# Kernel tuning notes

Hardware: AMD Instinct MI355X
Metric: run time of the kernel (lower is better)

## Reference

```python
import jax, jax.numpy as jnp
import numpy as np

B, C, H, W = 16, 256, 32, 32
N_HEAD, DIM_HEAD = 8, 32  # dim_hidden = 256 == C


def setup_inputs() -> dict:
    key = jax.random.key(0)
    ks = jax.random.split(key, 9)
    s = 1.0 / np.sqrt(C)
    return {
        "x": jax.random.normal(ks[0], (B, C, H, W), dtype=jnp.float32),
        "w_q": jax.random.normal(ks[1], (C, C), dtype=jnp.float32) * s,
        "b_q": jnp.zeros((C,), dtype=jnp.float32),
        "w_k": jax.random.normal(ks[2], (C, C), dtype=jnp.float32) * s,
        "b_k": jnp.zeros((C,), dtype=jnp.float32),
        "w_v": jax.random.normal(ks[3], (C, C), dtype=jnp.float32) * s,
        "b_v": jnp.zeros((C,), dtype=jnp.float32),
        "w_o": jax.random.normal(ks[4], (C, C), dtype=jnp.float32) * s,
        "b_o": jnp.zeros((C,), dtype=jnp.float32),
    }


def reference(x, w_q, b_q, w_k, b_k, w_v, b_v, w_o, b_o):
    b, c, h, w = x.shape
    L = h * w
    scale = DIM_HEAD ** (-0.5)
    xf = x.reshape(b, c, L)  # [b, c, L]

    def proj(wm, bm):
        # 1x1 conv == per-position linear over channels
        y = jnp.einsum('oc,bcl->bol', wm, xf) + bm[None, :, None]
        return y.reshape(b, N_HEAD, DIM_HEAD, L)

    q = proj(w_q, b_q) * scale
    k = proj(w_k, b_k)
    v = proj(w_v, b_v)

    sim = jnp.einsum('bndl,bndm->bnlm', q, k)           # [b, n, L, L]
    att = jax.nn.softmax(sim, axis=-1)
    out = jnp.einsum('bnlm,bndm->bndl', att, v)         # [b, n, d, L]
    out = out.reshape(b, c, L)
    out = jnp.einsum('oc,bcl->bol', w_o, out) + b_o[None, :, None]
    return out.reshape(b, c, h, w)
```

## Files before the change

### kernel.cpp

```cpp
#include <hip/hip_runtime.h>
#include <hip/hip_bf16.h>
#include <math.h>

namespace {
constexpr int B_ = 16, C_ = 256, L_ = 1024, NH_ = 8, DH_ = 32;

typedef __attribute__((ext_vector_type(8))) short short8v;
typedef __attribute__((ext_vector_type(4))) float float4v;

__device__ __forceinline__ short f2bf(float f) {
    unsigned u = __builtin_bit_cast(unsigned, f);
    u += 0x7fffu + ((u >> 16) & 1u);
    return (short)(u >> 16);
}
__device__ __forceinline__ unsigned pkrn(float a, float b) {
    float2 f; f.x = a; f.y = b;
    __hip_bfloat162 h = __float22bfloat162_rn(f);
    unsigned u;
    __builtin_memcpy(&u, &h, sizeof(u));
    return u;
}
__device__ __forceinline__ void gld16(const short* g, short* l) {
    __builtin_amdgcn_global_load_lds(
        (const __attribute__((address_space(1))) unsigned*)g,
        (__attribute__((address_space(3))) unsigned*)l, 16, 0, 0);
}

__global__ __launch_bounds__(256) void prepw_kernel(
    const float* __restrict__ wq, const float* __restrict__ wk,
    const float* __restrict__ wv, const float* __restrict__ wo,
    short* __restrict__ WA, short* __restrict__ WoA)
{
    const int g4 = blockIdx.x * 256 + threadIdx.x;
    const int o = g4 >> 6, cc = (g4 & 63) * 4;
    const float* src = (o < 256) ? wq : (o < 512) ? wk : (o < 768) ? wv : wo;
    const float4 v = *(const float4*)&src[(size_t)(o & 255) * 256 + cc];
    short4 s;
    s.x = f2bf(v.x); s.y = f2bf(v.y); s.z = f2bf(v.z); s.w = f2bf(v.w);
    short* dst = (o < 768) ? &WA[(size_t)o * 256 + cc]
                           : &WoA[(size_t)(o - 768) * 256 + cc];
    *(short4*)dst = s;
}

__global__ __launch_bounds__(256, 3) void qkv_kernel(
    const float* __restrict__ X, const short* __restrict__ WA,
    const float* __restrict__ bias0, const float* __restrict__ bias1, const float* __restrict__ bias2,
    float qscale, short* __restrict__ out0, short* __restrict__ out1, short* __restrict__ out2)
{
    const int lt = blockIdx.x, typ = blockIdx.y, b = blockIdx.z;
    const int t = threadIdx.x, wv = t >> 6, lane = t & 63;
    const int quad = lane >> 4, c = lane & 15;
    const int wo = (wv & 1) * 128;
    const int wl = (wv >> 1) * 32;

    __shared__ short sA[256 * 64];
    __shared__ short sB[64 * 64];

    float4v acc[8][2];
#pragma unroll
    for (int i = 0; i < 8; ++i)
#pragma unroll
        for (int j = 0; j < 2; ++j) acc[i][j] = (float4v)0.f;

    const short* Arow = WA + (size_t)(typ * 256) * 256;
    const int srow = t >> 3, sseg = t & 7;
    const int seg = sseg ^ (srow & 7);

    for (int kk = 0; kk < 4; ++kk) {
        __syncthreads();
#pragma unroll
        for (int e = 0; e < 8; ++e)
            gld16(Arow + (size_t)(e * 32 + srow) * 256 + kk * 64 + seg * 8,
                  &sA[(e * 256 + t) * 8]);
        {
            const int lrow = t & 63, w8 = t >> 6;
            const float* xcol = X + ((size_t)b * C_ + kk * 64 + w8 * 16) * L_ + lt * 64 + lrow;
            float vvv[16];
#pragma unroll
            for (int j = 0; j < 16; ++j) vvv[j] = xcol[(size_t)j * L_];
            unsigned pk[8];
#pragma unroll
            for (int j = 0; j < 8; ++j) pk[j] = pkrn(vvv[2 * j], vvv[2 * j + 1]);
            *(uint4*)&sB[(lrow * 8 + ((2 * w8)     ^ (lrow & 7))) * 8] = *(uint4*)&pk[0];
            *(uint4*)&sB[(lrow * 8 + ((2 * w8 + 1) ^ (lrow & 7))) * 8] = *(uint4*)&pk[4];
        }
        __syncthreads();

#pragma unroll
        for (int kc2 = 0; kc2 < 2; ++kc2) {
            short8v bf[2];
#pragma unroll
            for (int j = 0; j < 2; ++j) {
                const int row = wl + 16 * j + c;
                bf[j] = *(const short8v*)&sB[row * 64 + (((kc2 * 4 + quad) ^ (c & 7)) * 8)];
            }
#pragma unroll
            for (int half = 0; half < 2; ++half) {
                short8v af[4];
#pragma unroll
                for (int i2 = 0; i2 < 4; ++i2) {
                    const int row = wo + (half * 4 + i2) * 16 + c;
                    af[i2] = *(const short8v*)&sA[row * 64 + (((kc2 * 4 + quad) ^ (c & 7)) * 8)];
                }
#pragma unroll
                for (int i2 = 0; i2 < 4; ++i2)
#pragma unroll
                    for (int j = 0; j < 2; ++j)
                        acc[half * 4 + i2][j] = __builtin_amdgcn_mfma_f32_16x16x32_bf16(
                            af[i2], bf[j], acc[half * 4 + i2][j], 0, 0, 0);
            }
        }
    }

    const float* bp = (typ == 0) ? bias0 : (typ == 1) ? bias1 : bias2;
    const float sc = (typ == 0) ? qscale : 1.f;
    short* outp = (typ == 0) ? out0 : (typ == 1) ? out1 : out2;
    if (typ < 2) {
#pragma unroll
        for (int i = 0; i < 8; ++i) {
            const int ch0 = wo + 16 * i + quad * 4;
            const int head = ch0 >> 5, d0 = ch0 & 31;
            float bias[4];
#pragma unroll
            for (int r = 0; r < 4; ++r) bias[r] = bp[ch0 + r];
#pragma unroll
            for (int j = 0; j < 2; ++j) {
                const int l = lt * 64 + wl + 16 * j + c;
                short4 sv;
                sv.x = f2bf((acc[i][j][0] + bias[0]) * sc);
                sv.y = f2bf((acc[i][j][1] + bias[1]) * sc);
                sv.z = f2bf((acc[i][j][2] + bias[2]) * sc);
                sv.w = f2bf((acc[i][j][3] + bias[3]) * sc);
                *(short4*)&outp[(((size_t)b * NH_ + head) * L_ + l) * 32 + d0] = sv;
            }
        }
    } else {
#pragma unroll
        for (int i = 0; i < 8; ++i)
#pragma unroll
            for (int r = 0; r < 4; ++r) {
                const int ch = wo + 16 * i + quad * 4 + r;
                const float bias = bp[ch];
#pragma unroll
                for (int j = 0; j < 2; ++j)
                    outp[((size_t)b * C_ + ch) * L_ + lt * 64 + wl + 16 * j + c] =
                        f2bf(acc[i][j][r] + bias);
            }
    }
}

__global__ __launch_bounds__(256, 4) void ogemm_kernel(
    const short* __restrict__ WoA,
    const short* __restrict__ Bsrc,
    const float* __restrict__ bias,
    float* __restrict__ out)
{
    const int lt = blockIdx.x, ot = blockIdx.y, b = blockIdx.z;
    const int t = threadIdx.x, wv = t >> 6, lane = t & 63;
    const int quad = lane >> 4, c = lane & 15;
    const int wo = (wv & 1) * 64;
    const int wl = (wv >> 1) * 32;

    __shared__ short sA[128 * 64];
    __shared__ short sB[64 * 64];

    float4v acc[4][2];
#pragma unroll
    for (int i = 0; i < 4; ++i)
#pragma unroll
        for (int j = 0; j < 2; ++j) acc[i][j] = (float4v)0.f;

    const short* Arow = WoA + (size_t)(ot * 128) * 256;
    const int srow = t >> 3, sseg = t & 7;
    const int seg = sseg ^ (srow & 7);

    for (int kk = 0; kk < 4; ++kk) {
        __syncthreads();
#pragma unroll
        for (int e = 0; e < 4; ++e)
            gld16(Arow + (size_t)(e * 32 + srow) * 256 + kk * 64 + seg * 8,
                  &sA[(e * 256 + t) * 8]);
#pragma unroll
        for (int e = 0; e < 2; ++e)
            gld16(Bsrc + ((size_t)b * L_ + lt * 64 + e * 32 + srow) * 256 + kk * 64 + seg * 8,
                  &sB[(e * 256 + t) * 8]);
        __syncthreads();

#pragma unroll
        for (int kc2 = 0; kc2 < 2; ++kc2) {
            short8v af[4], bf[2];
#pragma unroll
            for (int i = 0; i < 4; ++i) {
                const int row = wo + 16 * i + c;
                af[i] = *(const short8v*)&sA[row * 64 + (((kc2 * 4 + quad) ^ (c & 7)) * 8)];
            }
#pragma unroll
            for (int j = 0; j < 2; ++j) {
                const int row = wl + 16 * j + c;
                bf[j] = *(const short8v*)&sB[row * 64 + (((kc2 * 4 + quad) ^ (c & 7)) * 8)];
            }
#pragma unroll
            for (int i = 0; i < 4; ++i)
#pragma unroll
                for (int j = 0; j < 2; ++j)
                    acc[i][j] = __builtin_amdgcn_mfma_f32_16x16x32_bf16(af[i], bf[j], acc[i][j], 0, 0, 0);
        }
    }

#pragma unroll
    for (int i = 0; i < 4; ++i)
#pragma unroll
        for (int r = 0; r < 4; ++r) {
            const int ch = ot * 128 + wo + 16 * i + quad * 4 + r;
            const float bs = bias[ch];
#pragma unroll
            for (int j = 0; j < 2; ++j)
                out[((size_t)b * C_ + ch) * L_ + lt * 64 + wl + 16 * j + c] =
                    acc[i][j][r] + bs;
        }
}

__global__ __launch_bounds__(256, 4) void attn_kernel(
    const short* __restrict__ qt,
    const short* __restrict__ kt,
    const short* __restrict__ vb,
    short* __restrict__ athi)
{
    const int flat = blockIdx.x;
    const int g = ((flat >> 6) << 3) | (flat & 7);
    const int chunk = (flat >> 3) & 7;
    const int b = g >> 3, h = g & 7;
    const int t = threadIdx.x;
    const int wv = t >> 6, lane = t & 63;
    const int quad = lane >> 4, c = lane & 15;
    const int lq0 = chunk * 128 + wv * 32;

    __shared__ __align__(16) short sK[2][64 * 32];
    __shared__ __align__(16) short sV[2][2][32 * 32];
    __shared__ __align__(16) short sPT[4][2][16][64];

    const size_t bh = (size_t)b * NH_ + h;
    const short* qbase = qt + (bh * L_) * 32;
    const short* kbase = kt + (bh * L_) * 32;
    const size_t vrow = (size_t)b * C_ + h * DH_;

    short8v qfrag[2];
#pragma unroll
    for (int qf = 0; qf < 2; ++qf)
        qfrag[qf] = *(const short8v*)(qbase + (size_t)(lq0 + qf * 16 + c) * 32 + quad * 8);

    float lp4[2][4];
#pragma unroll
    for (int qf = 0; qf < 2; ++qf)
#pragma unroll
        for (int r = 0; r < 4; ++r) lp4[qf][r] = 0.f;
    float4v o_acc[2][2];
#pragma unroll
    for (int qf = 0; qf < 2; ++qf) { o_acc[qf][0] = (float4v)0.f; o_acc[qf][1] = (float4v)0.f; }

    const int sseg = (t & 3) ^ ((t >> 3) & 3);
    const int rsw = (c >> 1) & 3;

    auto stage = [&](int m0, int buf) {
        gld16(kbase + (size_t)(m0 + (t >> 2)) * 32 + sseg * 8, &sK[buf][t * 8]);
        gld16(vb + (vrow + ((t >> 2) & 31)) * L_ + m0 + (t >> 7) * 32 + sseg * 8,
              (short*)sV[buf] + t * 8);
    };

    stage(0, 0);

    short8v vfp[2][2];

    for (int i = 0; i <= 16; ++i) {
        short8v kf[4], vf[2][2];
        if (i < 16) {
            __syncthreads();
            if (i < 15) stage((i + 1) * 64, (i + 1) & 1);
            const short* Kb = sK[i & 1];
            const short* Vb = (const short*)sV[i & 1];
#pragma unroll
            for (int kb = 0; kb < 4; ++kb)
                kf[kb] = *(const short8v*)&Kb[(kb * 16 + c) * 32 + ((quad ^ rsw) * 8)];
#pragma unroll
            for (int kc = 0; kc < 2; ++kc)
#pragma unroll
                for (int nb2 = 0; nb2 < 2; ++nb2)
                    vf[kc][nb2] = *(const short8v*)&Vb[kc * 1024 + (nb2 * 16 + c) * 32 + ((quad ^ rsw) * 8)];
        }

        if (i > 0) {
#pragma unroll
            for (int qf = 0; qf < 2; ++qf)
#pragma unroll
                for (int kc = 0; kc < 2; ++kc) {
                    const int G = (kc * 4 + quad) ^ (c & 7);
                    const short8v pf = *(const short8v*)&sPT[wv][qf][c][G * 8];
#pragma unroll
                    for (int nb2 = 0; nb2 < 2; ++nb2)
                        o_acc[qf][nb2] = __builtin_amdgcn_mfma_f32_16x16x32_bf16(vfp[kc][nb2], pf, o_acc[qf][nb2], 0, 0, 0);
                }
        }

        if (i < 16) {
            float4v st[2][4];
#pragma unroll
            for (int qf = 0; qf < 2; ++qf)
#pragma unroll
                for (int kb = 0; kb < 4; ++kb)
                    st[qf][kb] = __builtin_amdgcn_mfma_f32_16x16x32_bf16(kf[kb], qfrag[qf], (float4v)0.f, 0, 0, 0);
#pragma unroll
            for (int qf = 0; qf < 2; ++qf)
#pragma unroll
                for (int kb = 0; kb < 4; ++kb) {
                    float p[4];
#pragma unroll
                    for (int r = 0; r < 4; ++r) {
                        p[r] = __builtin_amdgcn_exp2f(st[qf][kb][r]);
                        lp4[qf][r] += p[r];
                    }
                    uint2 w;
                    w.x = pkrn(p[0], p[1]);
                    w.y = pkrn(p[2], p[3]);
                    const int Gw = (kb * 2 + (quad >> 1)) ^ (c & 7);
                    *(uint2*)&sPT[wv][qf][c][Gw * 8 + (quad & 1) * 4] = w;
                }
#pragma unroll
            for (int kc = 0; kc < 2; ++kc)
#pragma unroll
                for (int nb2 = 0; nb2 < 2; ++nb2) vfp[kc][nb2] = vf[kc][nb2];
        }
    }

#pragma unroll
    for (int qf = 0; qf < 2; ++qf) {
        float l = (lp4[qf][0] + lp4[qf][1]) + (lp4[qf][2] + lp4[qf][3]);
        l += __shfl_xor(l, 16);
        l += __shfl_xor(l, 32);
        const float inv = 1.f / l;
#pragma unroll
        for (int nb2 = 0; nb2 < 2; ++nb2) {
            short4 sv;
            sv.x = f2bf(o_acc[qf][nb2][0] * inv);
            sv.y = f2bf(o_acc[qf][nb2][1] * inv);
            sv.z = f2bf(o_acc[qf][nb2][2] * inv);
            sv.w = f2bf(o_acc[qf][nb2][3] * inv);
            *(short4*)&athi[((size_t)b * L_ + lq0 + qf * 16 + c) * C_ + h * DH_ + nb2 * 16 + quad * 4] = sv;
        }
    }
}

}

extern "C" void kernel_launch(void* const* d_in, const int* in_sizes, int n_in,
                              void* d_out, int out_size, void* d_ws, size_t ws_size,
                              hipStream_t stream) {
    const float* x   = (const float*)d_in[0];
    const float* w_q = (const float*)d_in[1];
    const float* b_q = (const float*)d_in[2];
    const float* w_k = (const float*)d_in[3];
    const float* b_k = (const float*)d_in[4];
    const float* w_v = (const float*)d_in[5];
    const float* b_v = (const float*)d_in[6];
    const float* w_o = (const float*)d_in[7];
    const float* b_o = (const float*)d_in[8];
    float* out = (float*)d_out;

    const size_t NT = (size_t)B_ * L_ * C_;
    short* WA   = (short*)d_ws;
    short* WoA  = WA + 768 * 256;
    short* qt   = WoA + 256 * 256;
    short* kt   = qt + NT;
    short* vb   = kt + NT;
    short* athi = vb + NT;

    const float scale_q = 0.17677669529663687f * 1.4426950408889634f;

    prepw_kernel<<<dim3(256), 256, 0, stream>>>(w_q, w_k, w_v, w_o, WA, WoA);
    qkv_kernel<<<dim3(L_ / 64, 3, B_), 256, 0, stream>>>(
        x, WA, b_q, b_k, b_v, scale_q, qt, kt, vb);
    attn_kernel<<<dim3(1024), 256, 0, stream>>>(qt, kt, vb, athi);
    ogemm_kernel<<<dim3(L_ / 64, 2, B_), 256, 0, stream>>>(
        WoA, athi, b_o, out);
}
```

Baseline: 134.4 us.

## Stage epilogue stores through LDS for coalesced writes; halve ogemm L-tile

The Q/K projection epilogue now transposes its tile through shared memory so each thread writes full 64-byte head rows with 16-byte stores instead of scattered 8-byte stores. The attention output is staged through the per-wave P buffer the same way. The output GEMM tile shrinks from 64 to 32 positions and the grid doubles, to raise occupancy and parallelism. The cost is extra LDS traffic, extra barriers, more blocks, and more reloads of the Wo tile.

```diff
diff --git a/kernel.cpp b/kernel.cpp
--- a/kernel.cpp
+++ b/kernel.cpp
@@ -53,8 +53,9 @@
     const int wo = (wv & 1) * 128;
     const int wl = (wv >> 1) * 32;
 
-    __shared__ short sA[256 * 64];
-    __shared__ short sB[64 * 64];
+    __shared__ short smem[20480];
+    short* sA = smem;
+    short* sB = smem + 16384;
 
     float4v acc[8][2];
 #pragma unroll
@@ -116,23 +117,35 @@
     const float sc = (typ == 0) ? qscale : 1.f;
     short* outp = (typ == 0) ? out0 : (typ == 1) ? out1 : out2;
     if (typ < 2) {
+        __syncthreads();
+        short* sT = smem;
 #pragma unroll
         for (int i = 0; i < 8; ++i) {
             const int ch0 = wo + 16 * i + quad * 4;
-            const int head = ch0 >> 5, d0 = ch0 & 31;
             float bias[4];
 #pragma unroll
             for (int r = 0; r < 4; ++r) bias[r] = bp[ch0 + r];
 #pragma unroll
             for (int j = 0; j < 2; ++j) {
-                const int l = lt * 64 + wl + 16 * j + c;
                 short4 sv;
                 sv.x = f2bf((acc[i][j][0] + bias[0]) * sc);
                 sv.y = f2bf((acc[i][j][1] + bias[1]) * sc);
                 sv.z = f2bf((acc[i][j][2] + bias[2]) * sc);
                 sv.w = f2bf((acc[i][j][3] + bias[3]) * sc);
-                *(short4*)&outp[(((size_t)b * NH_ + head) * L_ + l) * 32 + d0] = sv;
-            }
+                *(short4*)&sT[(wl + 16 * j + c) * 264 + ch0] = sv;
+            }
+        }
+        __syncthreads();
+#pragma unroll
+        for (int k = 0; k < 2; ++k) {
+            const int u = k * 256 + t;
+            const int h = u >> 6, l = u & 63;
+            const short* src = &sT[l * 264 + h * 32];
+            short* dst = &outp[(((size_t)b * NH_ + h) * L_ + lt * 64 + l) * 32];
+            *(uint4*)&dst[0]  = *(const uint4*)&src[0];
+            *(uint4*)&dst[8]  = *(const uint4*)&src[8];
+            *(uint4*)&dst[16] = *(const uint4*)&src[16];
+            *(uint4*)&dst[24] = *(const uint4*)&src[24];
         }
     } else {
 #pragma unroll
@@ -159,16 +172,14 @@
     const int t = threadIdx.x, wv = t >> 6, lane = t & 63;
     const int quad = lane >> 4, c = lane & 15;
     const int wo = (wv & 1) * 64;
-    const int wl = (wv >> 1) * 32;
+    const int wl = (wv >> 1) * 16;
 
     __shared__ short sA[128 * 64];
-    __shared__ short sB[64 * 64];
-
-    float4v acc[4][2];
-#pragma unroll
-    for (int i = 0; i < 4; ++i)
-#pragma unroll
-        for (int j = 0; j < 2; ++j) acc[i][j] = (float4v)0.f;
+    __shared__ short sB[32 * 64];
+
+    float4v acc[4];
+#pragma unroll
+    for (int i = 0; i < 4; ++i) acc[i] = (float4v)0.f;
 
     const short* Arow = WoA + (size_t)(ot * 128) * 256;
     const int srow = t >> 3, sseg = t & 7;
@@ -180,30 +191,25 @@
         for (int e = 0; e < 4; ++e)
             gld16(Arow + (size_t)(e * 32 + srow) * 256 + kk * 64 + seg * 8,
                   &sA[(e * 256 + t) * 8]);
-#pragma unroll
-        for (int e = 0; e < 2; ++e)
-            gld16(Bsrc + ((size_t)b * L_ + lt * 64 + e * 32 + srow) * 256 + kk * 64 + seg * 8,
-                  &sB[(e * 256 + t) * 8]);
+        gld16(Bsrc + ((size_t)b * L_ + lt * 32 + srow) * 256 + kk * 64 + seg * 8,
+              &sB[t * 8]);
         __syncthreads();
 
 #pragma unroll
         for (int kc2 = 0; kc2 < 2; ++kc2) {
-            short8v af[4], bf[2];
+            short8v af[4], bf;
 #pragma unroll
             for (int i = 0; i < 4; ++i) {
                 const int row = wo + 16 * i + c;
                 af[i] = *(const short8v*)&sA[row * 64 + (((kc2 * 4 + quad) ^ (c & 7)) * 8)];
             }
-#pragma unroll
-            for (int j = 0; j < 2; ++j) {
-                const int row = wl + 16 * j + c;
-                bf[j] = *(const short8v*)&sB[row * 64 + (((kc2 * 4 + quad) ^ (c & 7)) * 8)];
+            {
+                const int row = wl + c;
+                bf = *(const short8v*)&sB[row * 64 + (((kc2 * 4 + quad) ^ (c & 7)) * 8)];
             }
 #pragma unroll
             for (int i = 0; i < 4; ++i)
-#pragma unroll
-                for (int j = 0; j < 2; ++j)
-                    acc[i][j] = __builtin_amdgcn_mfma_f32_16x16x32_bf16(af[i], bf[j], acc[i][j], 0, 0, 0);
+                acc[i] = __builtin_amdgcn_mfma_f32_16x16x32_bf16(af[i], bf, acc[i], 0, 0, 0);
         }
     }
 
@@ -212,11 +218,7 @@
 #pragma unroll
         for (int r = 0; r < 4; ++r) {
             const int ch = ot * 128 + wo + 16 * i + quad * 4 + r;
-            const float bs = bias[ch];
-#pragma unroll
-            for (int j = 0; j < 2; ++j)
-                out[((size_t)b * C_ + ch) * L_ + lt * 64 + wl + 16 * j + c] =
-                    acc[i][j][r] + bs;
+            out[((size_t)b * C_ + ch) * L_ + lt * 32 + wl + c] = acc[i][r] + bias[ch];
         }
 }
 
@@ -331,6 +333,7 @@
         }
     }
 
+    short* sW = (short*)&sPT[wv][0][0][0];
 #pragma unroll
     for (int qf = 0; qf < 2; ++qf) {
         float l = (lp4[qf][0] + lp4[qf][1]) + (lp4[qf][2] + lp4[qf][3]);
@@ -344,8 +347,15 @@
             sv.y = f2bf(o_acc[qf][nb2][1] * inv);
             sv.z = f2bf(o_acc[qf][nb2][2] * inv);
             sv.w = f2bf(o_acc[qf][nb2][3] * inv);
-            *(short4*)&athi[((size_t)b * L_ + lq0 + qf * 16 + c) * C_ + h * DH_ + nb2 * 16 + quad * 4] = sv;
-        }
+            *(short4*)&sW[(qf * 16 + c) * 40 + nb2 * 16 + quad * 4] = sv;
+        }
+    }
+    {
+        const int lq = lane & 31, hf = lane >> 5;
+        const short* src = &sW[lq * 40 + hf * 16];
+        short* dst = &athi[((size_t)b * L_ + lq0 + lq) * C_ + h * DH_ + hf * 16];
+        *(uint4*)&dst[0] = *(const uint4*)&src[0];
+        *(uint4*)&dst[8] = *(const uint4*)&src[8];
     }
 }
 
@@ -379,6 +389,6 @@
     qkv_kernel<<<dim3(L_ / 64, 3, B_), 256, 0, stream>>>(
         x, WA, b_q, b_k, b_v, scale_q, qt, kt, vb);
     attn_kernel<<<dim3(1024), 256, 0, stream>>>(qt, kt, vb, athi);
-    ogemm_kernel<<<dim3(L_ / 64, 2, B_), 256, 0, stream>>>(
+    ogemm_kernel<<<dim3(L_ / 32, 2, B_), 256, 0, stream>>>(
         WoA, athi, b_o, out);
 }
```

Result: slower. 137.6 us (+2.4%).
